# Kernel tuning notes

Measured on AMD Instinct MI355X. Metric: run time of the kernel, lower is better.

The kernel has to match this reference:

```python
import jax, jax.numpy as jnp
import numpy as np

B, CIN, COUT, N = 64, 1024, 1024, 49   # batch, in_features, out_features, flattened spatial
GROUPS = 1
CHUNK = 16                              # output-channel tile to bound intermediate memory


def setup_inputs() -> dict:
    key = jax.random.key(0)
    k1, k2 = jax.random.split(key)
    x = jax.random.normal(k1, (B, CIN, N), dtype=jnp.float32)
    weight = jax.random.normal(k2, (COUT, CIN // GROUPS), dtype=jnp.float32)  # std=1.0 init
    bias = jnp.zeros((COUT,), dtype=jnp.float32)
    return {"x": x, "weight": weight, "bias": bias}


def norm_dist_inf(x, weight, groups, chunk):
    # x: [B, Cin, N], weight: [Cout, Cin//groups]
    # out[b, o, n] = max_d |x[b, g(o)*d + d', n] - weight[o, d']|  (L-inf distance)
    Bb, Cin, Nn = x.shape
    Cout, d = weight.shape
    og = Cout // groups
    xg = x.reshape(Bb, groups, d, Nn)                 # [B, g, d, N]
    wg = weight.reshape(groups, og, d)                # [g, og, d]
    # tile output channels to avoid materializing [B, Cout, Cin, N]
    wchunks = wg.reshape(groups, og // chunk, chunk, d).transpose(1, 0, 2, 3)  # [nc, g, chunk, d]

    def body(carry, wc):
        # diff: [B, g, chunk, d, N] -> max over d
        out = jnp.max(jnp.abs(xg[:, :, None, :, :] - wc[None, :, :, :, None]), axis=3)
        return carry, out                              # [B, g, chunk, N]

    _, outs = jax.lax.scan(body, None, wchunks)        # [nc, B, g, chunk, N]
    out = outs.transpose(1, 2, 0, 3, 4).reshape(Bb, Cout, Nn)
    return out


def reference(x, weight, bias):
    out = norm_dist_inf(x, weight, GROUPS, CHUNK)      # [B, Cout, N]
    return out + bias[None, :, None]
```

## Files before the change

kernel.cpp:

```cpp
#include <hip/hip_runtime.h>


typedef float v2f __attribute__((ext_vector_type(2)));
typedef float v4f __attribute__((ext_vector_type(4)));

constexpr int CIN  = 1024;
constexpr int COUT = 1024;
constexpr int NN   = 49;
constexpr int BB   = 64;
constexpr int P    = BB * NN;
constexpr int CPW  = 8;
constexpr int WPB  = 2;
constexpr int CPB  = CPW * WPB;
constexpr int NT   = CIN / 4;

#define PKSUB(d, wp, xp) \
    asm("v_pk_add_f32 %0, %1, %2 neg_lo:[0,1] neg_hi:[0,1]" \
        : "=v"(d) : "s"(wp), "v"(xp))
#define AMAX3(a, lo, hi) \
    asm("v_max3_f32 %0, %0, |%1|, |%2|" : "+v"(a) : "v"(lo), "v"(hi))

__global__ __launch_bounds__(128) void ndist_kernel(
    const float* __restrict__ x, const float* __restrict__ w,
    const float* __restrict__ bias, float* __restrict__ out)
{
    const int lane = threadIdx.x & 63;
    const int wid  = __builtin_amdgcn_readfirstlane(threadIdx.x >> 6);

    const int p = blockIdx.y * BB + lane;
    const int b = p / NN;
    const int n = p - b * NN;
    const int o0 = blockIdx.x * CPB + wid * CPW;

    const float* __restrict__ xrow = x + (size_t)b * CIN * NN + n;
    const float* __restrict__ wb   = w + (size_t)o0 * CIN;

    float acc[CPW];
#pragma unroll
    for (int c = 0; c < CPW; ++c) acc[c] = 0.0f;

    v2f xA[2], xB[2];
    v2f wA[CPW][2], wB[CPW][2];

#define LOAD_X(dst, kt) do {                                   \
        float _x0 = xrow[((kt) * 4 + 0) * NN];                 \
        float _x1 = xrow[((kt) * 4 + 1) * NN];                 \
        float _x2 = xrow[((kt) * 4 + 2) * NN];                 \
        float _x3 = xrow[((kt) * 4 + 3) * NN];                 \
        dst[0] = (v2f){_x0, _x1};                              \
        dst[1] = (v2f){_x2, _x3};                              \
    } while (0)

#define LOAD_W(dst, kt) do {                                   \
        _Pragma("unroll")                                      \
        for (int c = 0; c < CPW; ++c) {                        \
            v4f t = *(const v4f*)(wb + (size_t)c * CIN + (kt) * 4); \
            dst[c][0] = (v2f){t.x, t.y};                       \
            dst[c][1] = (v2f){t.z, t.w};                       \
        }                                                      \
    } while (0)

#define COMPUTE(xv, wv) do {                                   \
        _Pragma("unroll")                                      \
        for (int c = 0; c < CPW; ++c) {                        \
            v2f d0, d1;                                        \
            PKSUB(d0, wv[c][0], xv[0]);                        \
            PKSUB(d1, wv[c][1], xv[1]);                        \
            AMAX3(acc[c], d0.x, d0.y);                         \
            AMAX3(acc[c], d1.x, d1.y);                         \
        }                                                      \
    } while (0)

    LOAD_X(xA, 0);
    LOAD_W(wA, 0);

    for (int kt = 0; kt < NT; kt += 2) {
        LOAD_X(xB, kt + 1);
        LOAD_W(wB, kt + 1);
        COMPUTE(xA, wA);

        const int ktn = (kt + 2) & (NT - 1);
        LOAD_X(xA, ktn);
        LOAD_W(wA, ktn);
        COMPUTE(xB, wB);
    }

#pragma unroll
    for (int c = 0; c < CPW; ++c) {
        const int o = o0 + c;
        out[((size_t)b * COUT + o) * NN + n] = acc[c] + bias[o];
    }
}

extern "C" void kernel_launch(void* const* d_in, const int* in_sizes, int n_in,
                              void* d_out, int out_size, void* d_ws, size_t ws_size,
                              hipStream_t stream) {
    const float* x    = (const float*)d_in[0];
    const float* w    = (const float*)d_in[1];
    const float* bias = (const float*)d_in[2];
    float* out        = (float*)d_out;

    dim3 grid(COUT / CPB, P / BB);
    ndist_kernel<<<grid, 128, 0, stream>>>(x, w, bias, out);
}
```

Before: 141.8 us.

## Repack weights into tiled layout and load them through VGPRs

```diff
diff --git a/kernel.cpp b/kernel.cpp
--- a/kernel.cpp
+++ b/kernel.cpp
@@ -16,12 +16,19 @@
 
 #define PKSUB(d, wp, xp) \
     asm("v_pk_add_f32 %0, %1, %2 neg_lo:[0,1] neg_hi:[0,1]" \
-        : "=v"(d) : "s"(wp), "v"(xp))
+        : "=v"(d) : "v"(wp), "v"(xp))
 #define AMAX3(a, lo, hi) \
     asm("v_max3_f32 %0, %0, |%1|, |%2|" : "+v"(a) : "v"(lo), "v"(hi))
 
+__global__ void pack_w_kernel(const float* __restrict__ w, float* __restrict__ wq) {
+    int idx = blockIdx.x * 256 + threadIdx.x;
+    int o = idx >> 10, k = idx & 1023;
+    int og = o >> 3, c = o & 7, kt = k >> 2, ku = k & 3;
+    wq[(((size_t)og * NT + kt) * 8 + c) * 4 + ku] = w[idx];
+}
+
 __global__ __launch_bounds__(128) void ndist_kernel(
-    const float* __restrict__ x, const float* __restrict__ w,
+    const float* __restrict__ x, const float* __restrict__ wq,
     const float* __restrict__ bias, float* __restrict__ out)
 {
     const int lane = threadIdx.x & 63;
@@ -30,17 +37,21 @@
     const int p = blockIdx.y * BB + lane;
     const int b = p / NN;
     const int n = p - b * NN;
-    const int o0 = blockIdx.x * CPB + wid * CPW;
+    const int og = blockIdx.x * WPB + wid;
+    const int o0 = og * CPW;
+
+    int lz;
+    asm("v_mov_b32 %0, 0" : "=v"(lz));
 
     const float* __restrict__ xrow = x + (size_t)b * CIN * NN + n;
-    const float* __restrict__ wb   = w + (size_t)o0 * CIN;
+    const float* __restrict__ wgp  = wq + (size_t)og * (NT * 32) + lz;
 
     float acc[CPW];
 #pragma unroll
     for (int c = 0; c < CPW; ++c) acc[c] = 0.0f;
 
+    v4f wA[CPW], wB[CPW];
     v2f xA[2], xB[2];
-    v2f wA[CPW][2], wB[CPW][2];
 
 #define LOAD_X(dst, kt) do {                                   \
         float _x0 = xrow[((kt) * 4 + 0) * NN];                 \
@@ -52,20 +63,19 @@
     } while (0)
 
 #define LOAD_W(dst, kt) do {                                   \
+        const v4f* _q = (const v4f*)(wgp + (size_t)(kt) * 32); \
         _Pragma("unroll")                                      \
-        for (int c = 0; c < CPW; ++c) {                        \
-            v4f t = *(const v4f*)(wb + (size_t)c * CIN + (kt) * 4); \
-            dst[c][0] = (v2f){t.x, t.y};                       \
-            dst[c][1] = (v2f){t.z, t.w};                       \
-        }                                                      \
+        for (int c = 0; c < CPW; ++c) dst[c] = _q[c];          \
     } while (0)
 
 #define COMPUTE(xv, wv) do {                                   \
         _Pragma("unroll")                                      \
         for (int c = 0; c < CPW; ++c) {                        \
+            v2f _lo = __builtin_shufflevector(wv[c], wv[c], 0, 1); \
+            v2f _hi = __builtin_shufflevector(wv[c], wv[c], 2, 3); \
             v2f d0, d1;                                        \
-            PKSUB(d0, wv[c][0], xv[0]);                        \
-            PKSUB(d1, wv[c][1], xv[1]);                        \
+            PKSUB(d0, _lo, xv[0]);                             \
+            PKSUB(d1, _hi, xv[1]);                             \
             AMAX3(acc[c], d0.x, d0.y);                         \
             AMAX3(acc[c], d1.x, d1.y);                         \
         }                                                      \
@@ -92,6 +102,44 @@
     }
 }
 
+__global__ __launch_bounds__(128) void ndist_fallback(
+    const float* __restrict__ x, const float* __restrict__ w,
+    const float* __restrict__ bias, float* __restrict__ out)
+{
+    const int lane = threadIdx.x & 63;
+    const int wid  = __builtin_amdgcn_readfirstlane(threadIdx.x >> 6);
+    const int p = blockIdx.y * BB + lane;
+    const int b = p / NN, n = p - b * NN;
+    const int o0 = blockIdx.x * CPB + wid * CPW;
+    const float* __restrict__ xrow = x + (size_t)b * CIN * NN + n;
+    const float* __restrict__ wb   = w + (size_t)o0 * CIN;
+
+    float acc[CPW];
+#pragma unroll
+    for (int c = 0; c < CPW; ++c) acc[c] = 0.0f;
+
+    for (int kt = 0; kt < NT; ++kt) {
+        v2f xv[2];
+        LOAD_X(xv, kt);
+#pragma unroll
+        for (int c = 0; c < CPW; ++c) {
+            v4f t = *(const v4f*)(wb + (size_t)c * CIN + kt * 4);
+            v2f lo = __builtin_shufflevector(t, t, 0, 1);
+            v2f hi = __builtin_shufflevector(t, t, 2, 3);
+            v2f d0, d1;
+            PKSUB(d0, lo, xv[0]);
+            PKSUB(d1, hi, xv[1]);
+            AMAX3(acc[c], d0.x, d0.y);
+            AMAX3(acc[c], d1.x, d1.y);
+        }
+    }
+#pragma unroll
+    for (int c = 0; c < CPW; ++c) {
+        const int o = o0 + c;
+        out[((size_t)b * COUT + o) * NN + n] = acc[c] + bias[o];
+    }
+}
+
 extern "C" void kernel_launch(void* const* d_in, const int* in_sizes, int n_in,
                               void* d_out, int out_size, void* d_ws, size_t ws_size,
                               hipStream_t stream) {
@@ -100,6 +148,13 @@
     const float* bias = (const float*)d_in[2];
     float* out        = (float*)d_out;
 
+    const size_t wq_bytes = (size_t)COUT * CIN * sizeof(float);
     dim3 grid(COUT / CPB, P / BB);
-    ndist_kernel<<<grid, 128, 0, stream>>>(x, w, bias, out);
+    if (ws_size >= wq_bytes) {
+        float* wqd = (float*)d_ws;
+        pack_w_kernel<<<(COUT * CIN) / 256, 256, 0, stream>>>(w, wqd);
+        ndist_kernel<<<grid, 128, 0, stream>>>(x, wqd, bias, out);
+    } else {
+        ndist_fallback<<<grid, 128, 0, stream>>>(x, w, bias, out);
+    }
 }
```

Measured after the change: 498.7 us. 3.52x slower.

## Stage weight tiles through double-buffered LDS instead of scalar global loads

Applied to the files above, without the earlier changes.

```diff
diff --git a/kernel.cpp b/kernel.cpp
--- a/kernel.cpp
+++ b/kernel.cpp
@@ -12,11 +12,14 @@
 constexpr int CPW  = 8;
 constexpr int WPB  = 2;
 constexpr int CPB  = CPW * WPB;
-constexpr int NT   = CIN / 4;
+constexpr int KC   = 64;
+constexpr int NCH  = CIN / KC;
+constexpr int TPC  = KC / 4;
+constexpr int NTL  = CIN / 4;
 
 #define PKSUB(d, wp, xp) \
     asm("v_pk_add_f32 %0, %1, %2 neg_lo:[0,1] neg_hi:[0,1]" \
-        : "=v"(d) : "s"(wp), "v"(xp))
+        : "=v"(d) : "v"(wp), "v"(xp))
 #define AMAX3(a, lo, hi) \
     asm("v_max3_f32 %0, %0, |%1|, |%2|" : "+v"(a) : "v"(lo), "v"(hi))
 
@@ -24,16 +27,25 @@
     const float* __restrict__ x, const float* __restrict__ w,
     const float* __restrict__ bias, float* __restrict__ out)
 {
-    const int lane = threadIdx.x & 63;
-    const int wid  = __builtin_amdgcn_readfirstlane(threadIdx.x >> 6);
+    __shared__ float ws[2][CPB * KC];
+
+    const int t    = threadIdx.x;
+    const int lane = t & 63;
+    const int wid  = __builtin_amdgcn_readfirstlane(t >> 6);
 
     const int p = blockIdx.y * BB + lane;
     const int b = p / NN;
     const int n = p - b * NN;
-    const int o0 = blockIdx.x * CPB + wid * CPW;
+    const int o0b = blockIdx.x * CPB;
+    const int o0  = o0b + wid * CPW;
 
     const float* __restrict__ xrow = x + (size_t)b * CIN * NN + n;
-    const float* __restrict__ wb   = w + (size_t)o0 * CIN;
+
+    const int sc = t >> 4;
+    const int sk = (t & 15) * 4;
+    const float* __restrict__ g0 = w + (size_t)(o0b + sc) * CIN + sk;
+    const float* __restrict__ g1 = g0 + (size_t)8 * CIN;
+    const int e0 = t * 4;
 
     float acc[CPW];
 #pragma unroll
@@ -51,12 +63,12 @@
         dst[1] = (v2f){_x2, _x3};                              \
     } while (0)
 
-#define LOAD_W(dst, kt) do {                                   \
+#define LOAD_WS(dst, wsb, j) do {                              \
         _Pragma("unroll")                                      \
         for (int c = 0; c < CPW; ++c) {                        \
-            v4f t = *(const v4f*)(wb + (size_t)c * CIN + (kt) * 4); \
-            dst[c][0] = (v2f){t.x, t.y};                       \
-            dst[c][1] = (v2f){t.z, t.w};                       \
+            v4f q = *(const v4f*)((wsb) + c * KC + (j) * 4);   \
+            dst[c][0] = __builtin_shufflevector(q, q, 0, 1);   \
+            dst[c][1] = __builtin_shufflevector(q, q, 2, 3);   \
         }                                                      \
     } while (0)
 
@@ -71,18 +83,45 @@
         }                                                      \
     } while (0)
 
+    {
+        v4f r0 = *(const v4f*)g0;
+        v4f r1 = *(const v4f*)g1;
+        *(v4f*)&ws[0][e0]       = r0;
+        *(v4f*)&ws[0][e0 + 512] = r1;
+    }
+    __syncthreads();
     LOAD_X(xA, 0);
-    LOAD_W(wA, 0);
 
-    for (int kt = 0; kt < NT; kt += 2) {
-        LOAD_X(xB, kt + 1);
-        LOAD_W(wB, kt + 1);
-        COMPUTE(xA, wA);
+    for (int ch = 0; ch < NCH; ++ch) {
+        const int buf = ch & 1;
+        const bool more = (ch + 1 < NCH);
 
-        const int ktn = (kt + 2) & (NT - 1);
-        LOAD_X(xA, ktn);
-        LOAD_W(wA, ktn);
-        COMPUTE(xB, wB);
+        v4f p0, p1;
+        if (more) {
+            p0 = *(const v4f*)(g0 + (ch + 1) * KC);
+            p1 = *(const v4f*)(g1 + (ch + 1) * KC);
+        }
+
+        const float* __restrict__ wsb = &ws[buf][wid * (CPW * KC)];
+        LOAD_WS(wA, wsb, 0);
+#pragma unroll
+        for (int j = 0; j < TPC; j += 2) {
+            const int tg = ch * TPC + j;
+            LOAD_X(xB, tg + 1);
+            LOAD_WS(wB, wsb, j + 1);
+            COMPUTE(xA, wA);
+            const int tn = (tg + 2) & (NTL - 1);
+            LOAD_X(xA, tn);
+            LOAD_WS(wA, wsb, (j + 2) & (TPC - 1));
+            COMPUTE(xB, wB);
+        }
+
+        if (more) {
+            float* d = &ws[buf ^ 1][0];
+            *(v4f*)&d[e0]       = p0;
+            *(v4f*)&d[e0 + 512] = p1;
+        }
+        __syncthreads();
     }
 
 #pragma unroll
```

Result: slower. 154.0 us (+8.6%).

## Process four pixels per thread to reuse weight loads across pixels

Applied to the files above, without the earlier changes.

```diff
diff --git a/kernel.cpp b/kernel.cpp
--- a/kernel.cpp
+++ b/kernel.cpp
@@ -7,12 +7,14 @@
 constexpr int CIN  = 1024;
 constexpr int COUT = 1024;
 constexpr int NN   = 49;
-constexpr int BB   = 64;
-constexpr int P    = BB * NN;
+constexpr int P    = 3136;
 constexpr int CPW  = 8;
 constexpr int WPB  = 2;
 constexpr int CPB  = CPW * WPB;
-constexpr int NT   = CIN / 4;
+constexpr int PIX  = 4;
+constexpr int PT   = 64 * PIX;
+constexpr int NPT  = (P + PT - 1) / PT;
+constexpr int NTL  = CIN / 4;
 
 #define PKSUB(d, wp, xp) \
     asm("v_pk_add_f32 %0, %1, %2 neg_lo:[0,1] neg_hi:[0,1]" \
@@ -27,68 +29,88 @@
     const int lane = threadIdx.x & 63;
     const int wid  = __builtin_amdgcn_readfirstlane(threadIdx.x >> 6);
 
-    const int p = blockIdx.y * BB + lane;
-    const int b = p / NN;
-    const int n = p - b * NN;
-    const int o0 = blockIdx.x * CPB + wid * CPW;
+    const int o0    = blockIdx.x * CPB + wid * CPW;
+    const int pbase = blockIdx.y * PT;
 
-    const float* __restrict__ xrow = x + (size_t)b * CIN * NN + n;
-    const float* __restrict__ wb   = w + (size_t)o0 * CIN;
+    int b[PIX], n[PIX];
+    const float* xp[PIX];
+#pragma unroll
+    for (int i = 0; i < PIX; ++i) {
+        const bool valid = (pbase + i * 64) < P;
+        const int  pi    = (valid ? pbase + i * 64 : pbase) + lane;
+        b[i]  = pi / NN;
+        n[i]  = pi - b[i] * NN;
+        xp[i] = x + (size_t)b[i] * (CIN * NN) + n[i];
+    }
 
-    float acc[CPW];
+    const float* __restrict__ wb = w + (size_t)o0 * CIN;
+
+    float acc[CPW][PIX];
 #pragma unroll
-    for (int c = 0; c < CPW; ++c) acc[c] = 0.0f;
+    for (int c = 0; c < CPW; ++c)
+#pragma unroll
+        for (int i = 0; i < PIX; ++i) acc[c][i] = 0.0f;
 
-    v2f xA[2], xB[2];
+    v2f xA[PIX][2], xB[PIX][2];
     v2f wA[CPW][2], wB[CPW][2];
 
-#define LOAD_X(dst, kt) do {                                   \
-        float _x0 = xrow[((kt) * 4 + 0) * NN];                 \
-        float _x1 = xrow[((kt) * 4 + 1) * NN];                 \
-        float _x2 = xrow[((kt) * 4 + 2) * NN];                 \
-        float _x3 = xrow[((kt) * 4 + 3) * NN];                 \
-        dst[0] = (v2f){_x0, _x1};                              \
-        dst[1] = (v2f){_x2, _x3};                              \
+#define LOAD_X(dst, kt) do {                                     \
+        _Pragma("unroll")                                        \
+        for (int i = 0; i < PIX; ++i) {                          \
+            float a0 = xp[i][((kt) * 4 + 0) * NN];               \
+            float a1 = xp[i][((kt) * 4 + 1) * NN];               \
+            float a2 = xp[i][((kt) * 4 + 2) * NN];               \
+            float a3 = xp[i][((kt) * 4 + 3) * NN];               \
+            dst[i][0] = (v2f){a0, a1};                           \
+            dst[i][1] = (v2f){a2, a3};                           \
+        }                                                        \
     } while (0)
 
-#define LOAD_W(dst, kt) do {                                   \
-        _Pragma("unroll")                                      \
-        for (int c = 0; c < CPW; ++c) {                        \
-            v4f t = *(const v4f*)(wb + (size_t)c * CIN + (kt) * 4); \
-            dst[c][0] = (v2f){t.x, t.y};                       \
-            dst[c][1] = (v2f){t.z, t.w};                       \
-        }                                                      \
+#define LOAD_W(dst, kt) do {                                     \
+        _Pragma("unroll")                                        \
+        for (int c = 0; c < CPW; ++c) {                          \
+            v4f t = *(const v4f*)(wb + (size_t)c * CIN + (size_t)(kt) * 4); \
+            dst[c][0] = (v2f){t.x, t.y};                         \
+            dst[c][1] = (v2f){t.z, t.w};                         \
+        }                                                        \
     } while (0)
 
-#define COMPUTE(xv, wv) do {                                   \
-        _Pragma("unroll")                                      \
-        for (int c = 0; c < CPW; ++c) {                        \
-            v2f d0, d1;                                        \
-            PKSUB(d0, wv[c][0], xv[0]);                        \
-            PKSUB(d1, wv[c][1], xv[1]);                        \
-            AMAX3(acc[c], d0.x, d0.y);                         \
-            AMAX3(acc[c], d1.x, d1.y);                         \
-        }                                                      \
+#define COMPUTE(xv, wv) do {                                     \
+        _Pragma("unroll")                                        \
+        for (int c = 0; c < CPW; ++c)                            \
+        _Pragma("unroll")                                        \
+        for (int i = 0; i < PIX; ++i) {                          \
+            v2f d0, d1;                                          \
+            PKSUB(d0, wv[c][0], xv[i][0]);                       \
+            PKSUB(d1, wv[c][1], xv[i][1]);                       \
+            AMAX3(acc[c][i], d0.x, d0.y);                        \
+            AMAX3(acc[c][i], d1.x, d1.y);                        \
+        }                                                        \
     } while (0)
 
+    LOAD_W(wA, 0);
     LOAD_X(xA, 0);
-    LOAD_W(wA, 0);
 
-    for (int kt = 0; kt < NT; kt += 2) {
+    for (int kt = 0; kt < NTL; kt += 2) {
+        LOAD_W(wB, kt + 1);
         LOAD_X(xB, kt + 1);
-        LOAD_W(wB, kt + 1);
         COMPUTE(xA, wA);
 
-        const int ktn = (kt + 2) & (NT - 1);
+        const int ktn = (kt + 2) & (NTL - 1);
+        LOAD_W(wA, ktn);
         LOAD_X(xA, ktn);
-        LOAD_W(wA, ktn);
         COMPUTE(xB, wB);
     }
 
 #pragma unroll
-    for (int c = 0; c < CPW; ++c) {
-        const int o = o0 + c;
-        out[((size_t)b * COUT + o) * NN + n] = acc[c] + bias[o];
+    for (int i = 0; i < PIX; ++i) {
+        if ((pbase + i * 64) < P) {
+#pragma unroll
+            for (int c = 0; c < CPW; ++c) {
+                const int o = o0 + c;
+                out[((size_t)b[i] * COUT + o) * NN + n[i]] = acc[c][i] + bias[o];
+            }
+        }
     }
 }
 
@@ -100,6 +122,6 @@
     const float* bias = (const float*)d_in[2];
     float* out        = (float*)d_out;
 
-    dim3 grid(COUT / CPB, P / BB);
+    dim3 grid(COUT / CPB, NPT);
     ndist_kernel<<<grid, 128, 0, stream>>>(x, w, bias, out);
 }
```

Result: slower. 180.0 us (+27.0%).
